# Kernel optimization log

Measured on AMD Instinct MI355X. Metric: run time of the kernel, lower is better.

The kernel has to match this reference:

```python
import jax, jax.numpy as jnp
import numpy as np

THRESHOLD = 0.7


def ternary_dequant(w, threshold=THRESHOLD):
    """Ternary quantize {-1,0,+1} with masked-mean alpha, return ternary*alpha."""
    abs_w = jnp.abs(w)
    delta = threshold * jnp.mean(abs_w)
    ternary = jnp.where(w > delta, 1.0, jnp.where(w < -delta, -1.0, 0.0)).astype(w.dtype)
    nz = ternary != 0
    cnt = jnp.sum(nz)
    # alpha = mean(|w| over nonzero ternary entries); fall back to mean(|w|) if all-zero
    masked_sum = jnp.sum(jnp.where(nz, abs_w, 0.0))
    alpha = jnp.where(cnt > 0, masked_sum / jnp.maximum(cnt, 1).astype(w.dtype), jnp.mean(abs_w))
    return ternary * alpha


def setup_inputs() -> dict:
    key = jax.random.key(0)
    kx, kw, kb = jax.random.split(key, 3)
    B, S, D_IN, D_OUT = 4, 2048, 4096, 4096
    x = jax.random.normal(kx, (B * S, D_IN), dtype=jnp.float32)
    # xavier-uniform-ish init for latent FP32 weights
    limit = np.sqrt(6.0 / (D_IN + D_OUT)).astype(np.float32)
    weight = jax.random.uniform(kw, (D_OUT, D_IN), dtype=jnp.float32, minval=-limit, maxval=limit)
    bias = jax.random.normal(kb, (D_OUT,), dtype=jnp.float32) * 0.02
    return {"x": x, "weight": weight, "bias": bias}


def reference(x, weight, bias):
    q_weight = ternary_dequant(weight)  # (out, in)
    return jnp.matmul(x, q_weight.T) + bias  # (tokens, out)
```

## Files before the change

kernel.cpp:

```cpp
#include <hip/hip_runtime.h>

#define M_DIM 8192
#define N_DIM 4096
#define K_DIM 4096

typedef __attribute__((ext_vector_type(8))) __bf16 bf16x8;
typedef __attribute__((ext_vector_type(4))) __bf16 bf16x4;
typedef __attribute__((ext_vector_type(4))) float floatx4;

__device__ __forceinline__ void async_copy16(const void* g, void* l) {
    __builtin_amdgcn_global_load_lds(
        (const __attribute__((address_space(1))) void*)g,
        (__attribute__((address_space(3))) void*)l,
        16, 0, 0);
}

__device__ __forceinline__ unsigned lds_addr(const void* p) {
    return (unsigned)(unsigned long long)(const __attribute__((address_space(3))) void*)p;
}
#define DSRD(dst, addr, OFF) \
    asm volatile("ds_read_b128 %0, %1 offset:" #OFF : "=v"(dst) : "v"(addr))

#define SB  __builtin_amdgcn_sched_barrier(0)
#define SP1 __builtin_amdgcn_s_setprio(1)
#define SP0 __builtin_amdgcn_s_setprio(0)

__device__ __forceinline__ double wave_reduce_d(double v) {
    #pragma unroll
    for (int o = 32; o > 0; o >>= 1) v += __shfl_down(v, o, 64);
    return v;
}
__device__ __forceinline__ unsigned wave_reduce_u(unsigned v) {
    #pragma unroll
    for (int o = 32; o > 0; o >>= 1) v += __shfl_down(v, o, 64);
    return v;
}

__global__ __launch_bounds__(256) void k_pre(const float4* __restrict__ w4,
                                             double* __restrict__ part,
                                             const float4* __restrict__ x4,
                                             bf16x4* __restrict__ xb) {
    const int tid = threadIdx.x;
    if (blockIdx.x < 2048) {
        int idx = blockIdx.x * 256 + tid;
        double s = 0.0;
        #pragma unroll
        for (int it = 0; it < 8; ++it) {
            float4 v = w4[idx + it * (2048 * 256)];
            s += (double)fabsf(v.x) + (double)fabsf(v.y) +
                 (double)fabsf(v.z) + (double)fabsf(v.w);
        }
        s = wave_reduce_d(s);
        __shared__ double sm[4];
        if ((tid & 63) == 0) sm[tid >> 6] = s;
        __syncthreads();
        if (tid == 0) part[blockIdx.x] = sm[0] + sm[1] + sm[2] + sm[3];
    } else {
        int idx = (blockIdx.x - 2048) * 256 + tid;
        #pragma unroll
        for (int it = 0; it < 4; ++it) {
            int i = idx + it * (8192 * 256);
            float4 v = x4[i];
            bf16x4 o;
            o[0] = (__bf16)v.x; o[1] = (__bf16)v.y;
            o[2] = (__bf16)v.z; o[3] = (__bf16)v.w;
            xb[i] = o;
        }
    }
}

__global__ __launch_bounds__(256) void k_quant(const float4* __restrict__ w4,
                                               bf16x4* __restrict__ tern,
                                               const double* __restrict__ part,
                                               double* __restrict__ scal,
                                               double* __restrict__ pm,
                                               unsigned* __restrict__ pc) {
    const int tid = threadIdx.x;
    double s = 0.0;
    #pragma unroll
    for (int i = 0; i < 8; ++i) s += part[tid + i * 256];
    s = wave_reduce_d(s);
    __shared__ double sm[4];
    if ((tid & 63) == 0) sm[tid >> 6] = s;
    __syncthreads();
    const double mean = (sm[0] + sm[1] + sm[2] + sm[3]) * (1.0 / 16777216.0);
    const double delta = 0.7 * mean;
    if (blockIdx.x == 0 && tid == 0) scal[0] = mean;

    int idx = blockIdx.x * 256 + tid;
    double msum = 0.0;
    unsigned cnt = 0;
    #pragma unroll
    for (int it = 0; it < 8; ++it) {
        int i = idx + it * (2048 * 256);
        float4 v = w4[i];
        float e[4] = {v.x, v.y, v.z, v.w};
        bf16x4 o;
        #pragma unroll
        for (int c = 0; c < 4; ++c) {
            float wv = e[c];
            float t = ((double)wv > delta) ? 1.0f
                    : (((double)wv < -delta) ? -1.0f : 0.0f);
            if (t != 0.0f) { msum += (double)fabsf(wv); cnt++; }
            o[c] = (__bf16)t;
        }
        tern[i] = o;
    }
    msum = wave_reduce_d(msum);
    cnt  = wave_reduce_u(cnt);
    __shared__ double smd[4];
    __shared__ unsigned smu[4];
    if ((tid & 63) == 0) { smd[tid >> 6] = msum; smu[tid >> 6] = cnt; }
    __syncthreads();
    if (tid == 0) {
        pm[blockIdx.x] = smd[0] + smd[1] + smd[2] + smd[3];
        pc[blockIdx.x] = smu[0] + smu[1] + smu[2] + smu[3];
    }
}

__global__ __launch_bounds__(512, 2) void ternary_gemm(
    const __bf16* __restrict__ A,
    const __bf16* __restrict__ B,
    const float*  __restrict__ bias,
    const double* __restrict__ scal,
    const double* __restrict__ pm,
    const unsigned* __restrict__ pc,
    float* __restrict__ C)
{
    __shared__ __attribute__((aligned(128))) __bf16 As[4][8192];
    __shared__ __attribute__((aligned(128))) __bf16 Bs[4][8192];
    __shared__ double smd[8];
    __shared__ unsigned smu[8];

    const int tid  = threadIdx.x;
    const int w    = tid >> 6;
    const int lane = tid & 63;
    const int quad = lane >> 4;
    const int l16  = lane & 15;
    const int wr = w >> 2;
    const int wc = w & 3;

    const int id = (blockIdx.x & 7) * 64 + (blockIdx.x >> 3);
    const int br = id >> 4;
    const int bc = id & 15;

    const int srow = lane >> 2;
    const int scol = ((lane & 3) ^ ((srow >> 1) & 3)) * 8;

    const __bf16* gA0 = A + (size_t)(br * 256 + (2 * w + 0) * 16 + srow) * K_DIM + scol;
    const __bf16* gA1 = A + (size_t)(br * 256 + (2 * w + 1) * 16 + srow) * K_DIM + scol;
    const __bf16* gB0 = B + (size_t)(bc * 256 + (2 * w + 0) * 16 + srow) * K_DIM + scol;
    const __bf16* gB1 = B + (size_t)(bc * 256 + (2 * w + 1) * 16 + srow) * K_DIM + scol;

    floatx4 acc[8][4] = {};

    const int swz   = (quad ^ ((l16 >> 1) & 3)) * 8;
    const int a_off = (wr * 128 + l16) * 64 + swz * 2;
    const int b_off = (wc * 64  + l16) * 64 + swz * 2;

    const unsigned aS0 = lds_addr(&As[0][0]) + (unsigned)a_off;
    const unsigned aS1 = aS0 + 16384;
    const unsigned aS2 = aS0 + 32768;
    const unsigned aS3 = aS0 + 49152;
    const unsigned bS0 = lds_addr(&Bs[0][0]) + (unsigned)b_off;
    const unsigned bS1 = bS0 + 16384;
    const unsigned bS2 = bS0 + 32768;
    const unsigned bS3 = bS0 + 49152;

    bf16x8 rA0[8], rA1[8], rB0[4], rB1[4];

#define STAGE2A(stg_, SLOT) do {                                   \
        const int _so = (stg_) * 32;                               \
        async_copy16(gA0 + _so, &As[SLOT][(2 * w + 0) * 512]);     \
        async_copy16(gA1 + _so, &As[SLOT][(2 * w + 1) * 512]);     \
    } while (0)
#define STAGE2B(stg_, SLOT) do {                                   \
        const int _so = (stg_) * 32;                               \
        async_copy16(gB0 + _so, &Bs[SLOT][(2 * w + 0) * 512]);     \
        async_copy16(gB1 + _so, &Bs[SLOT][(2 * w + 1) * 512]);     \
    } while (0)

#define MF4(CUR, I) do {                                                        \
        acc[I][0] = __builtin_amdgcn_mfma_f32_16x16x32_bf16(rA##CUR[I], rB##CUR[0], acc[I][0], 0, 0, 0); \
        acc[I][1] = __builtin_amdgcn_mfma_f32_16x16x32_bf16(rA##CUR[I], rB##CUR[1], acc[I][1], 0, 0, 0); \
        acc[I][2] = __builtin_amdgcn_mfma_f32_16x16x32_bf16(rA##CUR[I], rB##CUR[2], acc[I][2], 0, 0, 0); \
        acc[I][3] = __builtin_amdgcn_mfma_f32_16x16x32_bf16(rA##CUR[I], rB##CUR[3], acc[I][3], 0, 0, 0); \
    } while (0)

#define ITER(AN, BN, SSLOT, CUR, NXT, stg_, VMN, DO_DSR, DO_STAGE) do {        \
        asm volatile("s_waitcnt vmcnt(" #VMN ")" ::: "memory");                \
        __builtin_amdgcn_s_barrier();                                          \
        asm volatile("s_waitcnt lgkmcnt(0)" ::: "memory");                     \
        SB;                                                                    \
        SP1; MF4(CUR, 0); SP0; SB;                                             \
        if (DO_DSR) { DSRD(rA##NXT[0], AN, 0);                                 \
                      DSRD(rA##NXT[1], AN, 1024);                              \
                      DSRD(rA##NXT[2], AN, 2048); }                            \
        SB;                                                                    \
        SP1; MF4(CUR, 1); SP0; SB;                                             \
        if (DO_DSR) { DSRD(rA##NXT[3], AN, 3072);                              \
                      DSRD(rB##NXT[0], BN, 0);                                 \
                      DSRD(rB##NXT[1], BN, 1024); }                            \
        SB;                                                                    \
        SP1; MF4(CUR, 2); SP0; SB;                                             \
        if (DO_DSR) { DSRD(rB##NXT[2], BN, 2048);                              \
                      DSRD(rB##NXT[3], BN, 3072);                              \
                      DSRD(rA##NXT[4], AN, 4096); }                            \
        SB;                                                                    \
        SP1; MF4(CUR, 3); SP0; SB;                                             \
        if (DO_DSR) { DSRD(rA##NXT[5], AN, 5120);                              \
                      DSRD(rA##NXT[6], AN, 6144);                              \
                      DSRD(rA##NXT[7], AN, 7168); }                            \
        SB;                                                                    \
        SP1; MF4(CUR, 4); SP0; SB;                                             \
        if (DO_STAGE) STAGE2A(stg_, SSLOT);                                    \
        SB;                                                                    \
        SP1; MF4(CUR, 5); SP0; SB;                                             \
        if (DO_STAGE) STAGE2B(stg_, SSLOT);                                    \
        SB;                                                                    \
        SP1; MF4(CUR, 6); MF4(CUR, 7); SP0;                                    \
        SB;                                                                    \
    } while (0)

    STAGE2A(0, 0); STAGE2B(0, 0);
    STAGE2A(1, 1); STAGE2B(1, 1);
    STAGE2A(2, 2); STAGE2B(2, 2);
    asm volatile("s_waitcnt vmcnt(8)" ::: "memory");
    __builtin_amdgcn_s_barrier();
    DSRD(rA0[0], aS0, 0);    DSRD(rA0[1], aS0, 1024);
    DSRD(rA0[2], aS0, 2048); DSRD(rA0[3], aS0, 3072);
    DSRD(rA0[4], aS0, 4096); DSRD(rA0[5], aS0, 5120);
    DSRD(rA0[6], aS0, 6144); DSRD(rA0[7], aS0, 7168);
    DSRD(rB0[0], bS0, 0);    DSRD(rB0[1], bS0, 1024);
    DSRD(rB0[2], bS0, 2048); DSRD(rB0[3], bS0, 3072);

    for (int n = 0; n < 124; n += 4) {
        ITER(aS1, bS1, 3, 0, 1, n + 3, 4, 1, 1);
        ITER(aS2, bS2, 0, 1, 0, n + 4, 4, 1, 1);
        ITER(aS3, bS3, 1, 0, 1, n + 5, 4, 1, 1);
        ITER(aS0, bS0, 2, 1, 0, n + 6, 4, 1, 1);
    }
    ITER(aS1, bS1, 3, 0, 1, 127, 4, 1, 1);
    ITER(aS2, bS2, 0, 1, 0, 0,   4, 1, 0);
    ITER(aS3, bS3, 0, 0, 1, 0,   0, 1, 0);
    ITER(aS0, bS0, 0, 1, 0, 0,   0, 0, 0);

#undef ITER
#undef MF4
#undef STAGE2A
#undef STAGE2B

    double s = 0.0; unsigned c = 0;
    #pragma unroll
    for (int i = 0; i < 4; ++i) { s += pm[tid + i * 512]; c += pc[tid + i * 512]; }
    s = wave_reduce_d(s);
    c = wave_reduce_u(c);
    if (lane == 0) { smd[w] = s; smu[w] = c; }
    __syncthreads();
    double ms = 0.0; unsigned ct = 0;
    #pragma unroll
    for (int i = 0; i < 8; ++i) { ms += smd[i]; ct += smu[i]; }
    const float alpha = (float)(ct > 0 ? ms / (double)ct : scal[0]);

    float bv[4];
    #pragma unroll
    for (int j = 0; j < 4; ++j)
        bv[j] = bias[bc * 256 + wc * 64 + j * 16 + l16];

    #pragma unroll
    for (int i = 0; i < 8; ++i) {
        const int row0 = br * 256 + wr * 128 + i * 16 + quad * 4;
        #pragma unroll
        for (int j = 0; j < 4; ++j) {
            const int col = bc * 256 + wc * 64 + j * 16 + l16;
            #pragma unroll
            for (int r = 0; r < 4; ++r)
                C[(size_t)(row0 + r) * N_DIM + col] = acc[i][j][r] * alpha + bv[j];
        }
    }
}

extern "C" void kernel_launch(void* const* d_in, const int* in_sizes, int n_in,
                              void* d_out, int out_size, void* d_ws, size_t ws_size,
                              hipStream_t stream) {
    const float* x    = (const float*)d_in[0];
    const float* w    = (const float*)d_in[1];
    const float* bias = (const float*)d_in[2];
    float* out = (float*)d_out;

    char* ws = (char*)d_ws;
    double*   d_scal = (double*)ws;
    double*   part   = (double*)(ws + 64);
    double*   pm     = (double*)(ws + 16448);
    unsigned* pc     = (unsigned*)(ws + 32832);
    __bf16*   xb     = (__bf16*)(ws + 65536);
    __bf16*   tern   = (__bf16*)(ws + 65536 + (size_t)M_DIM * K_DIM * 2);

    k_pre<<<10240, 256, 0, stream>>>((const float4*)w, part, (const float4*)x, (bf16x4*)xb);
    k_quant<<<2048, 256, 0, stream>>>((const float4*)w, (bf16x4*)tern, part, d_scal, pm, pc);

    ternary_gemm<<<512, 512, 0, stream>>>(xb, tern, bias, d_scal, pm, pc, out);
}
```

Baseline: 618.8 us.

## Restructure GEMM main loop into two half-tile MFMA phases with extra barriers

Replaces the per-iteration interleave of eight MFMA groups with LDS reads and staging by a two-phase scheme. Each phase runs 16 MFMAs on half of the A fragments, and the high-half A reads, the async global stages and the next-slot low-half reads are issued between the phases. Register fragments are split into low/high A and B buffers, and several workgroup barriers and new lgkmcnt waits are added. The aim is a different overlap of LDS traffic with MFMA work and fewer live registers. The extra barriers and coarser interleaving may add stalls.

```diff
diff --git a/kernel.cpp b/kernel.cpp
--- a/kernel.cpp
+++ b/kernel.cpp
@@ -158,16 +158,16 @@
     const int a_off = (wr * 128 + l16) * 64 + swz * 2;
     const int b_off = (wc * 64  + l16) * 64 + swz * 2;
 
-    const unsigned aS0 = lds_addr(&As[0][0]) + (unsigned)a_off;
-    const unsigned aS1 = aS0 + 16384;
-    const unsigned aS2 = aS0 + 32768;
-    const unsigned aS3 = aS0 + 49152;
-    const unsigned bS0 = lds_addr(&Bs[0][0]) + (unsigned)b_off;
-    const unsigned bS1 = bS0 + 16384;
-    const unsigned bS2 = bS0 + 32768;
-    const unsigned bS3 = bS0 + 49152;
-
-    bf16x8 rA0[8], rA1[8], rB0[4], rB1[4];
+    const unsigned aR0 = lds_addr(&As[0][0]) + (unsigned)a_off;
+    const unsigned aR1 = aR0 + 16384;
+    const unsigned aR2 = aR0 + 32768;
+    const unsigned aR3 = aR0 + 49152;
+    const unsigned bR0 = lds_addr(&Bs[0][0]) + (unsigned)b_off;
+    const unsigned bR1 = bR0 + 16384;
+    const unsigned bR2 = bR0 + 32768;
+    const unsigned bR3 = bR0 + 49152;
+
+    bf16x8 aL0[4], aL1[4], aH0[4], aH1[4], bb0[4], bb1[4];
 
 #define STAGE2A(stg_, SLOT) do {                                   \
         const int _so = (stg_) * 32;                               \
@@ -180,46 +180,39 @@
         async_copy16(gB1 + _so, &Bs[SLOT][(2 * w + 1) * 512]);     \
     } while (0)
 
-#define MF4(CUR, I) do {                                                        \
-        acc[I][0] = __builtin_amdgcn_mfma_f32_16x16x32_bf16(rA##CUR[I], rB##CUR[0], acc[I][0], 0, 0, 0); \
-        acc[I][1] = __builtin_amdgcn_mfma_f32_16x16x32_bf16(rA##CUR[I], rB##CUR[1], acc[I][1], 0, 0, 0); \
-        acc[I][2] = __builtin_amdgcn_mfma_f32_16x16x32_bf16(rA##CUR[I], rB##CUR[2], acc[I][2], 0, 0, 0); \
-        acc[I][3] = __builtin_amdgcn_mfma_f32_16x16x32_bf16(rA##CUR[I], rB##CUR[3], acc[I][3], 0, 0, 0); \
-    } while (0)
-
-#define ITER(AN, BN, SSLOT, CUR, NXT, stg_, VMN, DO_DSR, DO_STAGE) do {        \
+#define MFQ(AF, BF, BASE) do {                                                 \
+        _Pragma("unroll")                                                      \
+        for (int i = 0; i < 4; ++i)                                            \
+            _Pragma("unroll")                                                  \
+            for (int j = 0; j < 4; ++j)                                        \
+                acc[(BASE) + i][j] = __builtin_amdgcn_mfma_f32_16x16x32_bf16(  \
+                    AF[i], BF[j], acc[(BASE) + i][j], 0, 0, 0);                \
+    } while (0)
+
+#define SLOT(AS, BS, AS2, BS2, P, Q, STG, SSLOT, VMN, DO_STAGE, DO_READ) do {  \
+             \
+        DSRD(aH##P[0], AS, 4096); DSRD(aH##P[1], AS, 5120);                    \
+        DSRD(aH##P[2], AS, 6144); DSRD(aH##P[3], AS, 7168);                    \
+        if (DO_STAGE) { STAGE2A(STG, SSLOT); STAGE2B(STG, SSLOT); }            \
         asm volatile("s_waitcnt vmcnt(" #VMN ")" ::: "memory");                \
         __builtin_amdgcn_s_barrier();                                          \
-        asm volatile("s_waitcnt lgkmcnt(0)" ::: "memory");                     \
+        asm volatile("s_waitcnt lgkmcnt(4)" ::: "memory");                     \
         SB;                                                                    \
-        SP1; MF4(CUR, 0); SP0; SB;                                             \
-        if (DO_DSR) { DSRD(rA##NXT[0], AN, 0);                                 \
-                      DSRD(rA##NXT[1], AN, 1024);                              \
-                      DSRD(rA##NXT[2], AN, 2048); }                            \
+        SP1; MFQ(aL##P, bb##P, 0); SP0; SB;                                    \
+        __builtin_amdgcn_s_barrier();                                          \
+              \
+        if (DO_READ) {                                                         \
+            DSRD(aL##Q[0], AS2, 0);    DSRD(aL##Q[1], AS2, 1024);              \
+            DSRD(aL##Q[2], AS2, 2048); DSRD(aL##Q[3], AS2, 3072);              \
+            DSRD(bb##Q[0], BS2, 0);    DSRD(bb##Q[1], BS2, 1024);              \
+            DSRD(bb##Q[2], BS2, 2048); DSRD(bb##Q[3], BS2, 3072);              \
+        }                                                                      \
+        __builtin_amdgcn_s_barrier();                                          \
+        if (DO_READ) { asm volatile("s_waitcnt lgkmcnt(8)" ::: "memory"); }    \
+        else         { asm volatile("s_waitcnt lgkmcnt(0)" ::: "memory"); }    \
         SB;                                                                    \
-        SP1; MF4(CUR, 1); SP0; SB;                                             \
-        if (DO_DSR) { DSRD(rA##NXT[3], AN, 3072);                              \
-                      DSRD(rB##NXT[0], BN, 0);                                 \
-                      DSRD(rB##NXT[1], BN, 1024); }                            \
-        SB;                                                                    \
-        SP1; MF4(CUR, 2); SP0; SB;                                             \
-        if (DO_DSR) { DSRD(rB##NXT[2], BN, 2048);                              \
-                      DSRD(rB##NXT[3], BN, 3072);                              \
-                      DSRD(rA##NXT[4], AN, 4096); }                            \
-        SB;                                                                    \
-        SP1; MF4(CUR, 3); SP0; SB;                                             \
-        if (DO_DSR) { DSRD(rA##NXT[5], AN, 5120);                              \
-                      DSRD(rA##NXT[6], AN, 6144);                              \
-                      DSRD(rA##NXT[7], AN, 7168); }                            \
-        SB;                                                                    \
-        SP1; MF4(CUR, 4); SP0; SB;                                             \
-        if (DO_STAGE) STAGE2A(stg_, SSLOT);                                    \
-        SB;                                                                    \
-        SP1; MF4(CUR, 5); SP0; SB;                                             \
-        if (DO_STAGE) STAGE2B(stg_, SSLOT);                                    \
-        SB;                                                                    \
-        SP1; MF4(CUR, 6); MF4(CUR, 7); SP0;                                    \
-        SB;                                                                    \
+        SP1; MFQ(aH##P, bb##P, 4); SP0; SB;                                    \
+        __builtin_amdgcn_s_barrier();                                          \
     } while (0)
 
     STAGE2A(0, 0); STAGE2B(0, 0);
@@ -227,26 +220,24 @@
     STAGE2A(2, 2); STAGE2B(2, 2);
     asm volatile("s_waitcnt vmcnt(8)" ::: "memory");
     __builtin_amdgcn_s_barrier();
-    DSRD(rA0[0], aS0, 0);    DSRD(rA0[1], aS0, 1024);
-    DSRD(rA0[2], aS0, 2048); DSRD(rA0[3], aS0, 3072);
-    DSRD(rA0[4], aS0, 4096); DSRD(rA0[5], aS0, 5120);
-    DSRD(rA0[6], aS0, 6144); DSRD(rA0[7], aS0, 7168);
-    DSRD(rB0[0], bS0, 0);    DSRD(rB0[1], bS0, 1024);
-    DSRD(rB0[2], bS0, 2048); DSRD(rB0[3], bS0, 3072);
-
-    for (int n = 0; n < 124; n += 4) {
-        ITER(aS1, bS1, 3, 0, 1, n + 3, 4, 1, 1);
-        ITER(aS2, bS2, 0, 1, 0, n + 4, 4, 1, 1);
-        ITER(aS3, bS3, 1, 0, 1, n + 5, 4, 1, 1);
-        ITER(aS0, bS0, 2, 1, 0, n + 6, 4, 1, 1);
-    }
-    ITER(aS1, bS1, 3, 0, 1, 127, 4, 1, 1);
-    ITER(aS2, bS2, 0, 1, 0, 0,   4, 1, 0);
-    ITER(aS3, bS3, 0, 0, 1, 0,   0, 1, 0);
-    ITER(aS0, bS0, 0, 1, 0, 0,   0, 0, 0);
-
-#undef ITER
-#undef MF4
+    DSRD(aL0[0], aR0, 0);    DSRD(aL0[1], aR0, 1024);
+    DSRD(aL0[2], aR0, 2048); DSRD(aL0[3], aR0, 3072);
+    DSRD(bb0[0], bR0, 0);    DSRD(bb0[1], bR0, 1024);
+    DSRD(bb0[2], bR0, 2048); DSRD(bb0[3], bR0, 3072);
+
+    for (int s = 0; s < 124; s += 4) {
+        SLOT(aR0, bR0, aR1, bR1, 0, 1, s + 3, 3, 8, 1, 1);
+        SLOT(aR1, bR1, aR2, bR2, 1, 0, s + 4, 0, 8, 1, 1);
+        SLOT(aR2, bR2, aR3, bR3, 0, 1, s + 5, 1, 8, 1, 1);
+        SLOT(aR3, bR3, aR0, bR0, 1, 0, s + 6, 2, 8, 1, 1);
+    }
+    SLOT(aR0, bR0, aR1, bR1, 0, 1, 127, 3, 8, 1, 1);
+    SLOT(aR1, bR1, aR2, bR2, 1, 0, 0,   0, 4, 0, 1);
+    SLOT(aR2, bR2, aR3, bR3, 0, 1, 0,   0, 0, 0, 1);
+    SLOT(aR3, bR3, aR0, bR0, 1, 0, 0,   0, 0, 0, 0);
+
+#undef SLOT
+#undef MFQ
 #undef STAGE2A
 #undef STAGE2B
 
```

New measurement: 547.3 us. -11.6%, faster.
